# Kernel tuning notes

Measured on AMD Instinct MI355X. Metric: run time of the kernel, lower is better.

## Reference

```python
import jax, jax.numpy as jnp
import numpy as np

B, H, S, D = 4, 16, 2048, 128


def setup_inputs() -> dict:
    key = jax.random.key(0)
    kq, kk, kv, km = jax.random.split(key, 4)
    query = jax.random.normal(kq, (B, H, S, D), dtype=jnp.float32)
    k = jax.random.normal(kk, (B, H, S, D), dtype=jnp.float32)
    value = jax.random.normal(kv, (B, H, S, D), dtype=jnp.float32)
    mask = jax.random.randint(km, (B, 1, S, S), 0, 2, dtype=jnp.int32)
    return {"query": query, "key": k, "value": value, "mask": mask, "softmax_dim": -1}


def reference(query, key, value, mask, softmax_dim):
    dk = query.shape[-1]
    # scores: [B, H, S, S]
    scores = jnp.einsum("bhqd,bhkd->bhqk", query, key) / jnp.sqrt(jnp.float32(dk))
    scores = jnp.where(mask == 0, jnp.float32(-1e9), scores)
    attention = jax.nn.softmax(scores, axis=softmax_dim)
    out = jnp.einsum("bhqk,bhkd->bhqd", attention, value)
    return (out, attention)
```

## Files before the change

### kernel.cpp

```cpp
#include <hip/hip_runtime.h>

typedef __attribute__((ext_vector_type(8))) short short8;
typedef __attribute__((ext_vector_type(4))) short short4v;
typedef __attribute__((ext_vector_type(4))) float float4v;

#define B_ 4
#define H_ 16
#define S_ 2048
#define D_ 128
#define BM 64
#define NKT64 32
#define NKT32 64

#define NSH (B_ * H_ * S_ * D_)
#define NMW ((size_t)B_ * 32 * S_)
#define WS_NEED (3ull * (unsigned long long)NSH * 2ull + (unsigned long long)NMW * 8ull)

#define QSCALE (0.08838834764831845f * 1.4426950408889634f)

__device__ __forceinline__ short f2bf(float f) {
  unsigned u = __float_as_uint(f);
  u = (u + 0x7fffu + ((u >> 16) & 1u)) >> 16;
  return (short)u;
}

__device__ __forceinline__ void gl16(const void* g, void* lds) {
  __builtin_amdgcn_global_load_lds(
      (const __attribute__((address_space(1))) unsigned int*)g,
      (__attribute__((address_space(3))) unsigned int*)lds, 16, 0, 0);
}

__global__ void prep_q(const float* __restrict__ Qg, short* __restrict__ Qb) {
  size_t id = (size_t)blockIdx.x * 256 + threadIdx.x;
  const float4v* src = (const float4v*)(Qg + id * 8);
  float4v a = src[0], b = src[1];
  short8 s;
  s[0] = f2bf(a[0] * QSCALE); s[1] = f2bf(a[1] * QSCALE);
  s[2] = f2bf(a[2] * QSCALE); s[3] = f2bf(a[3] * QSCALE);
  s[4] = f2bf(b[0] * QSCALE); s[5] = f2bf(b[1] * QSCALE);
  s[6] = f2bf(b[2] * QSCALE); s[7] = f2bf(b[3] * QSCALE);
  *((short8*)Qb + id) = s;
}

__global__ void prep_k(const float* __restrict__ Kg, short* __restrict__ Kf) {
  size_t id = (size_t)blockIdx.x * 256 + threadIdx.x;
  int c  = (int)(id & 15);
  int g  = (int)((id >> 4) & 3);
  int dc = (int)((id >> 6) & 3);
  int kf = (int)((id >> 8) & 3);
  int kt = (int)((id >> 10) & 31);
  size_t bh = id >> 15;
  const float* src = Kg + ((bh * S_ + (size_t)(kt * 64 + kf * 16 + c)) * D_) + dc * 32 + g * 8;
  float4v a = *(const float4v*)src;
  float4v b = *(const float4v*)(src + 4);
  short8 s;
  s[0] = f2bf(a[0]); s[1] = f2bf(a[1]); s[2] = f2bf(a[2]); s[3] = f2bf(a[3]);
  s[4] = f2bf(b[0]); s[5] = f2bf(b[1]); s[6] = f2bf(b[2]); s[7] = f2bf(b[3]);
  *((short8*)Kf + id) = s;
}

__global__ void prep_v(const float* __restrict__ Vg, short* __restrict__ Vf) {
  size_t id = (size_t)blockIdx.x * 256 + threadIdx.x;
  int c   = (int)(id & 15);
  int g   = (int)((id >> 4) & 3);
  int df  = (int)((id >> 6) & 7);
  int kt32= (int)((id >> 9) & 63);
  size_t bh = id >> 15;
  const float* src = Vg + (bh * S_ + (size_t)(kt32 * 32 + g * 8)) * D_ + df * 16 + c;
  short8 s;
#pragma unroll
  for (int e = 0; e < 8; ++e) s[e] = f2bf(src[(size_t)e * D_]);
  *((short8*)Vf + id) = s;
}

__global__ void prep_m(const int* __restrict__ Mg, unsigned long long* __restrict__ Bits) {
  int gw = blockIdx.x * 4 + (threadIdx.x >> 6);
  int j  = threadIdx.x & 63;
  int kt = gw & 31;
  int q  = (gw >> 5) & (S_ - 1);
  int b  = gw >> 16;
  int m = Mg[((size_t)b * S_ + q) * S_ + kt * 64 + j];
  unsigned long long bal = __ballot(m != 0);
  if (j == 0) Bits[((size_t)b * 32 + kt) * S_ + q] = bal;
}

__global__ __launch_bounds__(256, 4) void sdpa_main(
    const short* __restrict__ Qb, const short* __restrict__ Kfr,
    const short* __restrict__ Vfr, const unsigned long long* __restrict__ Bits,
    float* __restrict__ Og, float* __restrict__ Ag) {

  __shared__ __align__(16) char smem[32768 + 5120];
  short (*Ps)[40] = (short (*)[40])(smem + 32768);

  const int t = threadIdx.x;
  const int w = t >> 6;
  const int l = t & 63;
  const int g = l >> 4;
  const int c = l & 15;

  const int bid = blockIdx.x;
  const int qt = bid & 31;
  const int h  = (bid >> 5) & 15;
  const int b  = bid >> 9;

  const int qbase  = qt * BM;
  const int qrow_l = w * 16 + c;
  const int qrow   = qbase + qrow_l;

  const size_t bhOff = (size_t)(b * H_ + h) * (S_ * D_);
  const short* Qp  = Qb  + bhOff;
  const short* Kp  = Kfr + bhOff;
  const short* Vp  = Vfr + bhOff;
  const unsigned long long* Bp = Bits + (size_t)b * 32 * S_;
  const unsigned* Bu = (const unsigned*)Bits;
  float* Op = Og + bhOff;
  float* Ap = Ag + (size_t)(b * H_ + h) * ((size_t)S_ * S_);

  short8 qf[4];
#pragma unroll
  for (int dc = 0; dc < 4; ++dc)
    qf[dc] = *(const short8*)(Qp + (size_t)qrow * D_ + dc * 32 + g * 8);

#pragma unroll
  for (int i = 0; i < 4; ++i) {
    int f = w * 4 + i;
    gl16(Kp + f * 512 + l * 8, smem + f * 1024);
  }
  __syncthreads();

  float ls0 = 0.f, ls1 = 0.f, ls2 = 0.f, ls3 = 0.f;
  int cur = 0;
  for (int kt = 0; kt < NKT64; ++kt) {
    if (kt < NKT64 - 1) {
      const short* src = Kp + (size_t)(kt + 1) * 8192;
      char* dst = smem + (cur ^ 1) * 16384;
#pragma unroll
      for (int i = 0; i < 4; ++i) {
        int f = w * 4 + i;
        gl16(src + f * 512 + l * 8, dst + f * 1024);
      }
    }
    unsigned long long mb = Bp[(size_t)kt * S_ + qrow];
    const char* kb = smem + cur * 16384;

    float4v acc[4];
#pragma unroll
    for (int kf = 0; kf < 4; ++kf) acc[kf] = (float4v){0.f, 0.f, 0.f, 0.f};
#pragma unroll
    for (int kf = 0; kf < 4; ++kf) {
#pragma unroll
      for (int dc = 0; dc < 4; ++dc) {
        short8 af = *(const short8*)(kb + (kf * 4 + dc) * 1024 + l * 16);
        acc[kf] = __builtin_amdgcn_mfma_f32_16x16x32_bf16(af, qf[dc], acc[kf], 0, 0, 0);
      }
    }
#pragma unroll
    for (int kf = 0; kf < 4; ++kf) {
      unsigned mg = (unsigned)(mb >> (kf * 16 + g * 4)) & 0xFu;
      float p0 = ((mg >> 0) & 1) ? __builtin_amdgcn_exp2f(acc[kf][0]) : 0.f;
      float p1 = ((mg >> 1) & 1) ? __builtin_amdgcn_exp2f(acc[kf][1]) : 0.f;
      float p2 = ((mg >> 2) & 1) ? __builtin_amdgcn_exp2f(acc[kf][2]) : 0.f;
      float p3 = ((mg >> 3) & 1) ? __builtin_amdgcn_exp2f(acc[kf][3]) : 0.f;
      if (kf == 0) ls0 += (p0 + p1) + (p2 + p3);
      else if (kf == 1) ls1 += (p0 + p1) + (p2 + p3);
      else if (kf == 2) ls2 += (p0 + p1) + (p2 + p3);
      else ls3 += (p0 + p1) + (p2 + p3);
    }
    __syncthreads();
    cur ^= 1;
  }
  float lsum = (ls0 + ls1) + (ls2 + ls3);
  lsum += __shfl_xor(lsum, 16);
  lsum += __shfl_xor(lsum, 32);
  const float rl = (lsum > 0.f) ? (1.0f / lsum) : 0.f;

#pragma unroll
  for (int i = 0; i < 2; ++i) {
    int f = w + 4 * i;
    gl16(Kp + f * 512 + l * 8, smem + f * 1024);
    gl16(Vp + f * 512 + l * 8, smem + 16384 + f * 1024);
  }
  __syncthreads();

  float4v acco[8];
#pragma unroll
  for (int df = 0; df < 8; ++df) acco[df] = (float4v){0.f, 0.f, 0.f, 0.f};

  cur = 0;
  for (int kt = 0; kt < NKT32; ++kt) {
    if (kt < NKT32 - 1) {
      const short* ks = Kp + (size_t)(kt + 1) * 4096;
      const short* vs = Vp + (size_t)(kt + 1) * 4096;
      char* kd = smem + (cur ^ 1) * 8192;
      char* vd = smem + 16384 + (cur ^ 1) * 8192;
#pragma unroll
      for (int i = 0; i < 2; ++i) {
        int f = w + 4 * i;
        gl16(ks + f * 512 + l * 8, kd + f * 1024);
        gl16(vs + f * 512 + l * 8, vd + f * 1024);
      }
    }
    unsigned mw = Bu[((size_t)(b * 32 + (kt >> 1)) * S_ + qrow) * 2 + (kt & 1)];
    const char* kb = smem + cur * 8192;
    const char* vb = smem + 16384 + cur * 8192;

    float4v acc[2];
#pragma unroll
    for (int kf = 0; kf < 2; ++kf) acc[kf] = (float4v){0.f, 0.f, 0.f, 0.f};
#pragma unroll
    for (int kf = 0; kf < 2; ++kf) {
#pragma unroll
      for (int dc = 0; dc < 4; ++dc) {
        short8 af = *(const short8*)(kb + (kf * 4 + dc) * 1024 + l * 16);
        acc[kf] = __builtin_amdgcn_mfma_f32_16x16x32_bf16(af, qf[dc], acc[kf], 0, 0, 0);
      }
    }

#pragma unroll
    for (int kf = 0; kf < 2; ++kf) {
      int k0 = kt * 32 + kf * 16 + g * 4;
      unsigned mg = (mw >> (kf * 16 + g * 4)) & 0xFu;
      float4v aw;
      short4v pb;
#pragma unroll
      for (int r = 0; r < 4; ++r) {
        float pn = ((mg >> r) & 1) ? __builtin_amdgcn_exp2f(acc[kf][r]) * rl : 0.f;
        aw[r] = pn;
        pb[r] = f2bf(pn);
      }
      __builtin_nontemporal_store(aw, (float4v*)(Ap + (size_t)qrow * S_ + k0));
      *(short4v*)&Ps[qrow_l][kf * 16 + g * 4] = pb;
    }

    {
      short8 pbf = *(const short8*)&Ps[qrow_l][g * 8];
#pragma unroll
      for (int df = 0; df < 8; ++df) {
        short8 vf = *(const short8*)(vb + df * 1024 + l * 16);
        acco[df] = __builtin_amdgcn_mfma_f32_16x16x32_bf16(vf, pbf, acco[df], 0, 0, 0);
      }
    }
    __syncthreads();
    cur ^= 1;
  }

#pragma unroll
  for (int df = 0; df < 8; ++df) {
    *(float4v*)(Op + (size_t)qrow * D_ + df * 16 + g * 4) = acco[df];
  }
}

#define LQK 136
#define LVT 72

__global__ __launch_bounds__(256, 3) void sdpa_fallback(
    const float* __restrict__ Qg, const float* __restrict__ Kg,
    const float* __restrict__ Vg, const int* __restrict__ Mg,
    float* __restrict__ Og, float* __restrict__ Ag) {

  __shared__ __align__(16) char smemf[17408 + 27648];
  short (*Ks)[LQK]  = (short (*)[LQK])(smemf);
  short (*Qs)[LQK]  = (short (*)[LQK])(smemf + 17408);
  short (*VTs)[LVT] = (short (*)[LVT])(smemf + 17408);
  short (*Psf)[LVT] = (short (*)[LVT])(smemf + 17408 + 18432);

  const int t = threadIdx.x;
  const int w = t >> 6;
  const int l = t & 63;
  const int g = l >> 4;
  const int c = l & 15;

  const int bid = blockIdx.x;
  const int qt = bid & 31;
  const int h  = (bid >> 5) & 15;
  const int b  = bid >> 9;

  const int qbase  = qt * BM;
  const int qrow_l = w * 16 + c;
  const int qrow   = qbase + qrow_l;

  const size_t bhOff = (size_t)(b * H_ + h) * (S_ * D_);
  const float* Qp = Qg + bhOff;
  const float* Kp = Kg + bhOff;
  const float* Vp = Vg + bhOff;
  const int*   Mp = Mg + (size_t)b * S_ * S_;
  float* Op = Og + bhOff;
  float* Ap = Ag + (size_t)(b * H_ + h) * ((size_t)S_ * S_);

#pragma unroll
  for (int i = 0; i < 8; ++i) {
    int idx = t + i * 256;
    int d4 = idx & 31, row = idx >> 5;
    float4v v = *(const float4v*)(Qp + (size_t)(qbase + row) * D_ + d4 * 4);
    short4v s;
    s[0] = f2bf(v[0] * QSCALE); s[1] = f2bf(v[1] * QSCALE);
    s[2] = f2bf(v[2] * QSCALE); s[3] = f2bf(v[3] * QSCALE);
    *(short4v*)&Qs[row][d4 * 4] = s;
  }
  __syncthreads();

  short8 qf[4];
#pragma unroll
  for (int dc = 0; dc < 4; ++dc)
    qf[dc] = *(const short8*)&Qs[qrow_l][dc * 32 + g * 8];

  float m_run = -1e30f, l_run = 0.f;
  for (int kt = 0; kt < 32; ++kt) {
    __syncthreads();
#pragma unroll
    for (int i = 0; i < 8; ++i) {
      int idx = t + i * 256;
      int d4 = idx & 31, row = idx >> 5;
      float4v v = *(const float4v*)(Kp + (size_t)(kt * 64 + row) * D_ + d4 * 4);
      short4v s;
      s[0] = f2bf(v[0]); s[1] = f2bf(v[1]); s[2] = f2bf(v[2]); s[3] = f2bf(v[3]);
      *(short4v*)&Ks[row][d4 * 4] = s;
    }
    __syncthreads();

    float4v acc[4];
#pragma unroll
    for (int kf = 0; kf < 4; ++kf) acc[kf] = (float4v){0.f, 0.f, 0.f, 0.f};
#pragma unroll
    for (int kf = 0; kf < 4; ++kf) {
#pragma unroll
      for (int dc = 0; dc < 4; ++dc) {
        short8 af = *(const short8*)&Ks[kf * 16 + c][dc * 32 + g * 8];
        acc[kf] = __builtin_amdgcn_mfma_f32_16x16x32_bf16(af, qf[dc], acc[kf], 0, 0, 0);
      }
    }

    float sv[4][4];
    float tmax = -1e30f;
#pragma unroll
    for (int kf = 0; kf < 4; ++kf) {
      int k0 = kt * 64 + kf * 16 + g * 4;
      const int4 mv = *(const int4*)(Mp + (size_t)qrow * S_ + k0);
      int mr[4] = {mv.x, mv.y, mv.z, mv.w};
#pragma unroll
      for (int r = 0; r < 4; ++r) {
        float x = acc[kf][r];
        x = (mr[r] == 0) ? -1e9f : x;
        sv[kf][r] = x;
        tmax = fmaxf(tmax, x);
      }
    }
    tmax = fmaxf(tmax, __shfl_xor(tmax, 16));
    tmax = fmaxf(tmax, __shfl_xor(tmax, 32));
    float newm = fmaxf(m_run, tmax);
    float tsum = 0.f;
#pragma unroll
    for (int kf = 0; kf < 4; ++kf)
#pragma unroll
      for (int r = 0; r < 4; ++r)
        tsum += __builtin_amdgcn_exp2f(sv[kf][r] - newm);
    tsum += __shfl_xor(tsum, 16);
    tsum += __shfl_xor(tsum, 32);
    l_run = l_run * __builtin_amdgcn_exp2f(m_run - newm) + tsum;
    m_run = newm;
  }

  const float rl = 1.0f / l_run;

  float4v acco[8];
#pragma unroll
  for (int df = 0; df < 8; ++df) acco[df] = (float4v){0.f, 0.f, 0.f, 0.f};

  for (int kt = 0; kt < 32; ++kt) {
    __syncthreads();
#pragma unroll
    for (int i = 0; i < 8; ++i) {
      int idx = t + i * 256;
      int d4 = idx & 31, row = idx >> 5;
      float4v v = *(const float4v*)(Kp + (size_t)(kt * 64 + row) * D_ + d4 * 4);
      short4v s;
      s[0] = f2bf(v[0]); s[1] = f2bf(v[1]); s[2] = f2bf(v[2]); s[3] = f2bf(v[3]);
      *(short4v*)&Ks[row][d4 * 4] = s;
    }
#pragma unroll
    for (int i = 0; i < 8; ++i) {
      int idx = t + i * 256;
      int d = idx & 127, kq = idx >> 7;
      const float* vp = Vp + (size_t)(kt * 64 + kq * 4) * D_ + d;
      short4v s;
      s[0] = f2bf(vp[0]); s[1] = f2bf(vp[D_]); s[2] = f2bf(vp[2 * D_]); s[3] = f2bf(vp[3 * D_]);
      *(short4v*)&VTs[d][kq * 4] = s;
    }
    __syncthreads();

    float4v acc[4];
#pragma unroll
    for (int kf = 0; kf < 4; ++kf) acc[kf] = (float4v){0.f, 0.f, 0.f, 0.f};
#pragma unroll
    for (int kf = 0; kf < 4; ++kf) {
#pragma unroll
      for (int dc = 0; dc < 4; ++dc) {
        short8 af = *(const short8*)&Ks[kf * 16 + c][dc * 32 + g * 8];
        acc[kf] = __builtin_amdgcn_mfma_f32_16x16x32_bf16(af, qf[dc], acc[kf], 0, 0, 0);
      }
    }

#pragma unroll
    for (int kf = 0; kf < 4; ++kf) {
      int k0 = kt * 64 + kf * 16 + g * 4;
      const int4 mv = *(const int4*)(Mp + (size_t)qrow * S_ + k0);
      int mr[4] = {mv.x, mv.y, mv.z, mv.w};
      float4v aw;
      short4v pb;
#pragma unroll
      for (int r = 0; r < 4; ++r) {
        float x = acc[kf][r];
        x = (mr[r] == 0) ? -1e9f : x;
        float pn = __builtin_amdgcn_exp2f(x - m_run) * rl;
        aw[r] = pn;
        pb[r] = f2bf(pn);
      }
      __builtin_nontemporal_store(aw, (float4v*)(Ap + (size_t)qrow * S_ + k0));
      *(short4v*)&Psf[qrow_l][kf * 16 + g * 4] = pb;
    }

#pragma unroll
    for (int kc = 0; kc < 2; ++kc) {
      short8 pbf = *(const short8*)&Psf[qrow_l][kc * 32 + g * 8];
#pragma unroll
      for (int df = 0; df < 8; ++df) {
        short8 vf = *(const short8*)&VTs[df * 16 + c][kc * 32 + g * 8];
        acco[df] = __builtin_amdgcn_mfma_f32_16x16x32_bf16(vf, pbf, acco[df], 0, 0, 0);
      }
    }
  }

#pragma unroll
  for (int df = 0; df < 8; ++df) {
    *(float4v*)(Op + (size_t)qrow * D_ + df * 16 + g * 4) = acco[df];
  }
}

extern "C" void kernel_launch(void* const* d_in, const int* in_sizes, int n_in,
                              void* d_out, int out_size, void* d_ws, size_t ws_size,
                              hipStream_t stream) {
  const float* Q = (const float*)d_in[0];
  const float* K = (const float*)d_in[1];
  const float* V = (const float*)d_in[2];
  const int*   M = (const int*)d_in[3];
  float* Out  = (float*)d_out;
  float* Attn = Out + (size_t)B_ * H_ * S_ * D_;

  if (ws_size >= WS_NEED) {
    short* Qb = (short*)d_ws;
    short* Kf = Qb + (size_t)NSH;
    short* Vf = Kf + (size_t)NSH;
    unsigned long long* Bits = (unsigned long long*)(Vf + (size_t)NSH);
    const int pgrid = NSH / 8 / 256;
    prep_q<<<dim3(pgrid), dim3(256), 0, stream>>>(Q, Qb);
    prep_k<<<dim3(pgrid), dim3(256), 0, stream>>>(K, Kf);
    prep_v<<<dim3(pgrid), dim3(256), 0, stream>>>(V, Vf);
    prep_m<<<dim3((unsigned)(NMW / 4)), dim3(256), 0, stream>>>(M, Bits);
    sdpa_main<<<dim3(B_ * H_ * (S_ / BM)), dim3(256), 0, stream>>>(Qb, Kf, Vf, Bits, Out, Attn);
  } else {
    sdpa_fallback<<<dim3(B_ * H_ * (S_ / BM)), dim3(256), 0, stream>>>(Q, K, V, M, Out, Attn);
  }
}
```

Measured before the change: 456.9 us.

## Fuse Q conversion into main kernel, use packed bf16 converts, remap blocks per XCD

Removes the separate prep_q kernel and converts Q to scaled bf16 directly inside sdpa_main, which saves one launch and a workspace round trip. Scalar bf16 rounding in the prep and main kernels is replaced by the hardware v_cvt_pk_bf16_f32 instruction. The softmax normalisation now folds log2(sum) into the exp2 argument instead of multiplying by a reciprocal. Blocks are remapped so that each XCD handles whole head groups for better L2 locality, and the output store becomes nontemporal. The risks are small numerical differences from the log-domain normalisation and from the hardware rounding mode.

After: 433.5 us. -5.1%, faster.

```diff
diff --git a/kernel.cpp b/kernel.cpp
--- a/kernel.cpp
+++ b/kernel.cpp
@@ -14,9 +14,15 @@
 
 #define NSH (B_ * H_ * S_ * D_)
 #define NMW ((size_t)B_ * 32 * S_)
-#define WS_NEED (3ull * (unsigned long long)NSH * 2ull + (unsigned long long)NMW * 8ull)
+#define WS_NEED (2ull * (unsigned long long)NSH * 2ull + (unsigned long long)NMW * 8ull)
 
 #define QSCALE (0.08838834764831845f * 1.4426950408889634f)
+
+__device__ __forceinline__ unsigned cvtpk(float lo, float hi) {
+  unsigned r;
+  asm("v_cvt_pk_bf16_f32 %0, %1, %2" : "=v"(r) : "v"(lo), "v"(hi));
+  return r;
+}
 
 __device__ __forceinline__ short f2bf(float f) {
   unsigned u = __float_as_uint(f);
@@ -28,18 +34,6 @@
   __builtin_amdgcn_global_load_lds(
       (const __attribute__((address_space(1))) unsigned int*)g,
       (__attribute__((address_space(3))) unsigned int*)lds, 16, 0, 0);
-}
-
-__global__ void prep_q(const float* __restrict__ Qg, short* __restrict__ Qb) {
-  size_t id = (size_t)blockIdx.x * 256 + threadIdx.x;
-  const float4v* src = (const float4v*)(Qg + id * 8);
-  float4v a = src[0], b = src[1];
-  short8 s;
-  s[0] = f2bf(a[0] * QSCALE); s[1] = f2bf(a[1] * QSCALE);
-  s[2] = f2bf(a[2] * QSCALE); s[3] = f2bf(a[3] * QSCALE);
-  s[4] = f2bf(b[0] * QSCALE); s[5] = f2bf(b[1] * QSCALE);
-  s[6] = f2bf(b[2] * QSCALE); s[7] = f2bf(b[3] * QSCALE);
-  *((short8*)Qb + id) = s;
 }
 
 __global__ void prep_k(const float* __restrict__ Kg, short* __restrict__ Kf) {
@@ -53,10 +47,12 @@
   const float* src = Kg + ((bh * S_ + (size_t)(kt * 64 + kf * 16 + c)) * D_) + dc * 32 + g * 8;
   float4v a = *(const float4v*)src;
   float4v b = *(const float4v*)(src + 4);
-  short8 s;
-  s[0] = f2bf(a[0]); s[1] = f2bf(a[1]); s[2] = f2bf(a[2]); s[3] = f2bf(a[3]);
-  s[4] = f2bf(b[0]); s[5] = f2bf(b[1]); s[6] = f2bf(b[2]); s[7] = f2bf(b[3]);
-  *((short8*)Kf + id) = s;
+  int4 s;
+  s.x = (int)cvtpk(a[0], a[1]);
+  s.y = (int)cvtpk(a[2], a[3]);
+  s.z = (int)cvtpk(b[0], b[1]);
+  s.w = (int)cvtpk(b[2], b[3]);
+  ((int4*)Kf)[id] = s;
 }
 
 __global__ void prep_v(const float* __restrict__ Vg, short* __restrict__ Vf) {
@@ -67,10 +63,15 @@
   int kt32= (int)((id >> 9) & 63);
   size_t bh = id >> 15;
   const float* src = Vg + (bh * S_ + (size_t)(kt32 * 32 + g * 8)) * D_ + df * 16 + c;
-  short8 s;
-#pragma unroll
-  for (int e = 0; e < 8; ++e) s[e] = f2bf(src[(size_t)e * D_]);
-  *((short8*)Vf + id) = s;
+  float f[8];
+#pragma unroll
+  for (int e = 0; e < 8; ++e) f[e] = src[(size_t)e * D_];
+  int4 s;
+  s.x = (int)cvtpk(f[0], f[1]);
+  s.y = (int)cvtpk(f[2], f[3]);
+  s.z = (int)cvtpk(f[4], f[5]);
+  s.w = (int)cvtpk(f[6], f[7]);
+  ((int4*)Vf)[id] = s;
 }
 
 __global__ void prep_m(const int* __restrict__ Mg, unsigned long long* __restrict__ Bits) {
@@ -85,7 +86,7 @@
 }
 
 __global__ __launch_bounds__(256, 4) void sdpa_main(
-    const short* __restrict__ Qb, const short* __restrict__ Kfr,
+    const float* __restrict__ Qg, const short* __restrict__ Kfr,
     const short* __restrict__ Vfr, const unsigned long long* __restrict__ Bits,
     float* __restrict__ Og, float* __restrict__ Ag) {
 
@@ -96,21 +97,22 @@
   const int w = t >> 6;
   const int l = t & 63;
   const int g = l >> 4;
-  const int c = l & 15;
-
-  const int bid = blockIdx.x;
-  const int qt = bid & 31;
-  const int h  = (bid >> 5) & 15;
-  const int b  = bid >> 9;
+
+  const int p    = blockIdx.x;
+  const int xcd  = p & 7;
+  const int slot = p >> 3;
+  const int grp  = ((slot >> 5) << 3) + xcd;
+  const int qt   = slot & 31;
+  const int h    = grp & 15;
+  const int b    = grp >> 4;
 
   const int qbase  = qt * BM;
-  const int qrow_l = w * 16 + c;
+  const int qrow_l = w * 16 + (l & 15);
   const int qrow   = qbase + qrow_l;
 
   const size_t bhOff = (size_t)(b * H_ + h) * (S_ * D_);
-  const short* Qp  = Qb  + bhOff;
-  const short* Kp  = Kfr + bhOff;
-  const short* Vp  = Vfr + bhOff;
+  const short* Kp = Kfr + bhOff;
+  const short* Vp = Vfr + bhOff;
   const unsigned long long* Bp = Bits + (size_t)b * 32 * S_;
   const unsigned* Bu = (const unsigned*)Bits;
   float* Op = Og + bhOff;
@@ -118,8 +120,17 @@
 
   short8 qf[4];
 #pragma unroll
-  for (int dc = 0; dc < 4; ++dc)
-    qf[dc] = *(const short8*)(Qp + (size_t)qrow * D_ + dc * 32 + g * 8);
+  for (int dc = 0; dc < 4; ++dc) {
+    const float* qsrc = Qg + bhOff + (size_t)qrow * D_ + dc * 32 + g * 8;
+    float4v a = *(const float4v*)qsrc;
+    float4v c4 = *(const float4v*)(qsrc + 4);
+    int4 s;
+    s.x = (int)cvtpk(a[0] * QSCALE, a[1] * QSCALE);
+    s.y = (int)cvtpk(a[2] * QSCALE, a[3] * QSCALE);
+    s.z = (int)cvtpk(c4[0] * QSCALE, c4[1] * QSCALE);
+    s.w = (int)cvtpk(c4[2] * QSCALE, c4[3] * QSCALE);
+    qf[dc] = *(short8*)&s;
+  }
 
 #pragma unroll
   for (int i = 0; i < 4; ++i) {
@@ -172,7 +183,7 @@
   float lsum = (ls0 + ls1) + (ls2 + ls3);
   lsum += __shfl_xor(lsum, 16);
   lsum += __shfl_xor(lsum, 32);
-  const float rl = (lsum > 0.f) ? (1.0f / lsum) : 0.f;
+  const float lg = (lsum > 0.f) ? __log2f(lsum) : 1e30f;
 
 #pragma unroll
   for (int i = 0; i < 2; ++i) {
@@ -221,15 +232,16 @@
       int k0 = kt * 32 + kf * 16 + g * 4;
       unsigned mg = (mw >> (kf * 16 + g * 4)) & 0xFu;
       float4v aw;
-      short4v pb;
 #pragma unroll
       for (int r = 0; r < 4; ++r) {
-        float pn = ((mg >> r) & 1) ? __builtin_amdgcn_exp2f(acc[kf][r]) * rl : 0.f;
-        aw[r] = pn;
-        pb[r] = f2bf(pn);
-      }
+        float arg = ((mg >> r) & 1) ? (acc[kf][r] - lg) : -1e30f;
+        aw[r] = __builtin_amdgcn_exp2f(arg);
+      }
+      int2 pb;
+      pb.x = (int)cvtpk(aw[0], aw[1]);
+      pb.y = (int)cvtpk(aw[2], aw[3]);
       __builtin_nontemporal_store(aw, (float4v*)(Ap + (size_t)qrow * S_ + k0));
-      *(short4v*)&Ps[qrow_l][kf * 16 + g * 4] = pb;
+      *(int2*)&Ps[qrow_l][kf * 16 + g * 4] = pb;
     }
 
     {
@@ -246,7 +258,7 @@
 
 #pragma unroll
   for (int df = 0; df < 8; ++df) {
-    *(float4v*)(Op + (size_t)qrow * D_ + df * 16 + g * 4) = acco[df];
+    __builtin_nontemporal_store(acco[df], (float4v*)(Op + (size_t)qrow * D_ + df * 16 + g * 4));
   }
 }
 
@@ -447,16 +459,15 @@
   float* Attn = Out + (size_t)B_ * H_ * S_ * D_;
 
   if (ws_size >= WS_NEED) {
-    short* Qb = (short*)d_ws;
-    short* Kf = Qb + (size_t)NSH;
+    short* Kf = (short*)d_ws;
     short* Vf = Kf + (size_t)NSH;
     unsigned long long* Bits = (unsigned long long*)(Vf + (size_t)NSH);
     const int pgrid = NSH / 8 / 256;
-    prep_q<<<dim3(pgrid), dim3(256), 0, stream>>>(Q, Qb);
     prep_k<<<dim3(pgrid), dim3(256), 0, stream>>>(K, Kf);
     prep_v<<<dim3(pgrid), dim3(256), 0, stream>>>(V, Vf);
     prep_m<<<dim3((unsigned)(NMW / 4)), dim3(256), 0, stream>>>(M, Bits);
-    sdpa_main<<<dim3(B_ * H_ * (S_ / BM)), dim3(256), 0, stream>>>(Qb, Kf, Vf, Bits, Out, Attn);
+    sdpa_main<<<dim3(B_ * H_ * (S_ / BM)), dim3(256), 0, stream>>>(
+        Q, Kf, Vf, Bits, Out, Attn);
   } else {
     sdpa_fallback<<<dim3(B_ * H_ * (S_ / BM)), dim3(256), 0, stream>>>(Q, K, V, M, Out, Attn);
   }
```
